# Performance work log

Measured on AMD Instinct MI355X. Metric: run time of the kernel, lower is better.

The kernel has to match this reference:

```python
import jax, jax.numpy as jnp
import numpy as np

DIM = 192
TDIM = 192
HEADS = 6
WS = (2, 7, 7)
SS = (1, 3, 3)
MLP_HID = 4 * DIM
RANK = DIM // 8
EPS = 1e-6


def _rel_pos_index(ws):
    wd, wh, ww = ws
    coords = np.stack(np.meshgrid(np.arange(wd), np.arange(wh), np.arange(ww), indexing='ij'))
    cf = coords.reshape(3, -1)
    rel = (cf[:, :, None] - cf[:, None, :]).transpose(1, 2, 0).astype(np.int64)
    rel[..., 0] += wd - 1
    rel[..., 1] += wh - 1
    rel[..., 2] += ww - 1
    rel[..., 0] *= (2 * wh - 1) * (2 * ww - 1)
    rel[..., 1] *= (2 * ww - 1)
    return rel.sum(-1)  # (N, N)


def _window_partition(x, ws):
    B, D, H, W, C = x.shape
    x = x.reshape(B, D // ws[0], ws[0], H // ws[1], ws[1], W // ws[2], ws[2], C)
    return x.transpose(0, 1, 3, 5, 2, 4, 6, 7).reshape(-1, ws[0] * ws[1] * ws[2], C)


def _window_reverse(w, ws, B, D, H, W):
    x = w.reshape(B, D // ws[0], H // ws[1], W // ws[2], ws[0], ws[1], ws[2], -1)
    return x.transpose(0, 1, 4, 2, 5, 3, 6, 7).reshape(B, D, H, W, -1)


def _ln(x):
    m = x.mean(-1, keepdims=True)
    v = ((x - m) ** 2).mean(-1, keepdims=True)
    return (x - m) * jax.lax.rsqrt(v + EPS)


def _compute_mask_np(Dp, Hp, Wp, ws, ss):
    img = np.zeros((1, Dp, Hp, Wp, 1), dtype=np.float32)
    cnt = 0
    for d in (slice(0, -ws[0]), slice(-ws[0], -ss[0]), slice(-ss[0], None)):
        for h in (slice(0, -ws[1]), slice(-ws[1], -ss[1]), slice(-ss[1], None)):
            for w in (slice(0, -ws[2]), slice(-ws[2], -ss[2]), slice(-ss[2], None)):
                img[:, d, h, w, :] = cnt
                cnt += 1
    x = img.reshape(1, Dp // ws[0], ws[0], Hp // ws[1], ws[1], Wp // ws[2], ws[2], 1)
    mw = x.transpose(0, 1, 3, 5, 2, 4, 6, 7).reshape(-1, ws[0] * ws[1] * ws[2])
    am = mw[:, None, :] - mw[:, :, None]
    return np.where(am != 0, np.float32(-100.0), np.float32(0.0))


def setup_inputs() -> dict:
    key = jax.random.key(0)
    ks = jax.random.split(key, 16)
    B, D, H, W, C = 1, 16, 64, 128, DIM
    Dp = D + (-D) % WS[0]
    Hp = H + (-H) % WS[1]
    Wp = W + (-W) % WS[2]
    s = 0.02
    bias_tab = (2 * WS[0] - 1) * (2 * WS[1] - 1) * (2 * WS[2] - 1)
    return {
        'x': jax.random.normal(ks[0], (B, D, H, W, C), jnp.float32),
        'mask_matrix': jnp.asarray(_compute_mask_np(Dp, Hp, Wp, WS, SS)),
        't': jax.random.normal(ks[1], (B, TDIM), jnp.float32),
        'w_qkv': jax.random.normal(ks[2], (C, 3 * C), jnp.float32) * s,
        'b_qkv': jnp.zeros((3 * C,), jnp.float32),
        'rel_bias': jax.random.normal(ks[3], (bias_tab, HEADS), jnp.float32) * s,
        'w_proj': jax.random.normal(ks[4], (C, C), jnp.float32) * s,
        'b_proj': jnp.zeros((C,), jnp.float32),
        'w1': jax.random.normal(ks[5], (C, MLP_HID), jnp.float32) * s,
        'b1': jnp.zeros((MLP_HID,), jnp.float32),
        'w2': jax.random.normal(ks[6], (MLP_HID, C), jnp.float32) * s,
        'b2': jnp.zeros((C,), jnp.float32),
        'wa1': jax.random.normal(ks[7], (TDIM, RANK), jnp.float32) * s,
        'wa2': jax.random.normal(ks[8], (RANK, 6 * C), jnp.float32) * s,
        'ba2': jax.random.normal(ks[9], (6 * C,), jnp.float32) * s,
    }


def reference(x, mask_matrix, t, w_qkv, b_qkv, rel_bias, w_proj, b_proj, w1, b1, w2, b2, wa1, wa2, ba2):
    B, D, H, W, C = x.shape
    hd = C // HEADS
    # AdaLN modulation params
    mod = (jax.nn.silu(t) @ wa1) @ wa2 + ba2  # (B, 6C)
    sh_msa, sc_msa, g_msa, sh_mlp, sc_mlp, g_mlp = jnp.split(mod, 6, axis=1)

    def modulate(y, sh, sc):
        return y * (1 + sc[:, None, None, None, :]) + sh[:, None, None, None, :]

    shortcut = x
    y = modulate(_ln(x), sh_msa, sc_msa)
    # pad to window multiples
    pad_d, pad_h, pad_w = (-D) % WS[0], (-H) % WS[1], (-W) % WS[2]
    y = jnp.pad(y, ((0, 0), (0, pad_d), (0, pad_h), (0, pad_w), (0, 0)))
    Dp, Hp, Wp = D + pad_d, H + pad_h, W + pad_w
    # cyclic shift
    y = jnp.roll(y, (-SS[0], -SS[1], -SS[2]), axis=(1, 2, 3))
    xw = _window_partition(y, WS)  # (B*nW, N, C)
    N = xw.shape[1]
    qkv = (xw @ w_qkv + b_qkv).reshape(-1, N, 3, HEADS, hd)
    q, k, v = qkv[:, :, 0], qkv[:, :, 1], qkv[:, :, 2]
    scale = hd ** -0.5
    attn = jnp.einsum('bnhd,bmhd->bhnm', q * scale, k)  # (B*nW, H, N, N)
    rpi = _rel_pos_index(WS)
    bias = rel_bias[rpi.reshape(-1)].reshape(N, N, HEADS).transpose(2, 0, 1)
    attn = attn + bias[None]
    nW = mask_matrix.shape[0]
    attn = attn.reshape(B, nW, HEADS, N, N) + mask_matrix[None, :, None]
    attn = jax.nn.softmax(attn, axis=-1).reshape(-1, HEADS, N, N)
    out = jnp.einsum('bhnm,bmhd->bnhd', attn, v).reshape(-1, N, C)
    out = out @ w_proj + b_proj
    y = _window_reverse(out, WS, B, Dp, Hp, Wp)
    y = jnp.roll(y, (SS[0], SS[1], SS[2]), axis=(1, 2, 3))
    y = y[:, :D, :H, :W, :]
    x1 = shortcut + g_msa[:, None, None, None, :] * y
    y2 = modulate(_ln(x1), sh_mlp, sc_mlp)
    h = jax.nn.gelu(y2 @ w1 + b1, approximate=False) @ w2 + b2
    return x1 + g_mlp[:, None, None, None, :] * h
```

## Files before the change

### kernel.cpp

```cpp
#include <hip/hip_runtime.h>
#include <hip/hip_bf16.h>

typedef __bf16 bf16x8 __attribute__((ext_vector_type(8)));
typedef float  f32x4  __attribute__((ext_vector_type(4)));
typedef unsigned int u32x4 __attribute__((ext_vector_type(4)));
typedef __attribute__((address_space(3))) unsigned int lds_u32;
typedef const __attribute__((address_space(1))) unsigned int glb_u32;

__device__ inline unsigned short f2bf(float f) {
    union { __hip_bfloat16 h; unsigned short u; } cv;
    cv.h = __float2bfloat16(f);
    return cv.u;
}
__device__ inline float bf2f(unsigned short u) {
    union { unsigned int i; float f; } c; c.i = ((unsigned int)u) << 16; return c.f;
}

__device__ inline bf16x8 load8(const unsigned short* p) {
    uint2 lo = *(const uint2*)(p);
    uint2 hi = *(const uint2*)(p + 16);
    u32x4 v; v[0] = lo.x; v[1] = lo.y; v[2] = hi.x; v[3] = hi.y;
    return __builtin_bit_cast(bf16x8, v);
}

__device__ inline bf16x8 load8s(const unsigned short* rowbase, int lg, int r3) {
    int b0 = ((((lg >> 1)    ) ^ r3) << 4) + ((lg & 1) << 3);
    int b1 = ((((lg >> 1) + 2) ^ r3) << 4) + ((lg & 1) << 3);
    uint2 lo = *(const uint2*)((const char*)rowbase + b0);
    uint2 hi = *(const uint2*)((const char*)rowbase + b1);
    u32x4 v; v[0] = lo.x; v[1] = lo.y; v[2] = hi.x; v[3] = hi.y;
    return __builtin_bit_cast(bf16x8, v);
}

__device__ inline f32x4 mfma16(bf16x8 a, bf16x8 b, f32x4 c) {
    return __builtin_amdgcn_mfma_f32_16x16x32_bf16(a, b, c, 0, 0, 0);
}

__device__ inline bool winmapT(int gg, int& T) {
    int win = gg / 98, n = gg % 98;
    int wdi = win / 190, rem = win % 190, whi = rem / 19, wwi = rem % 19;
    int td = n / 49, th = (n / 7) % 7, tw = n % 7;
    int sd = (wdi * 2 + td + 1) & 15;
    int sh = whi * 7 + th + 3; if (sh >= 70) sh -= 70;
    int sw = wwi * 7 + tw + 3; if (sw >= 133) sw -= 133;
    if (sh < 64 && sw < 128) { T = (sd * 64 + sh) * 128 + sw; return true; }
    return false;
}

__device__ inline int xcd_swz(int orig, int nwg) {
    int q = nwg >> 3, r = nwg & 7;
    int xcd = orig & 7, idx = orig >> 3;
    return (xcd < r ? xcd * (q + 1) : r * (q + 1) + (xcd - r) * q) + idx;
}

__global__ __launch_bounds__(256) void mod_k(const float* __restrict__ t,
    const float* __restrict__ wa1, const float* __restrict__ wa2,
    const float* __restrict__ ba2, float* __restrict__ mod)
{
    __shared__ float st[192];
    __shared__ float a[24];
    int tid = threadIdx.x;
    if (tid < 192) { float x = t[tid]; st[tid] = x / (1.f + __expf(-x)); }
    __syncthreads();
    if (tid < 24) {
        float s = 0.f;
        for (int c = 0; c < 192; ++c) s += st[c] * wa1[c * 24 + tid];
        a[tid] = s;
    }
    __syncthreads();
    for (int j = tid; j < 1152; j += 256) {
        float s = ba2[j];
        for (int r = 0; r < 24; ++r) s += a[r] * wa2[r * 1152 + j];
        mod[j] = s;
    }
}

__global__ __launch_bounds__(256) void prep_k(
    const float* __restrict__ wqkv, const float* __restrict__ wproj,
    const float* __restrict__ w1, const float* __restrict__ w2,
    const float* __restrict__ relb,
    unsigned short* __restrict__ wqkvT, unsigned short* __restrict__ wprojT,
    unsigned short* __restrict__ w1T, unsigned short* __restrict__ w2T,
    unsigned short* __restrict__ btabF)
{
    int i = blockIdx.x * 256 + threadIdx.x;
    if (i < 110592) { int n = i / 192, k = i % 192; wqkvT[i] = f2bf(wqkv[k * 576 + n]); return; }
    i -= 110592;
    if (i < 36864)  { int n = i / 192, k = i % 192; wprojT[i] = f2bf(wproj[k * 192 + n]); return; }
    i -= 36864;
    if (i < 147456) { int n = i / 192, k = i % 192; w1T[i] = f2bf(w1[k * 768 + n]); return; }
    i -= 147456;
    if (i < 147456) { int n = i / 768, k = i % 768; w2T[i] = f2bf(w2[k * 192 + n]); return; }
    i -= 147456;
    if (i < 688128) {
        int mt = i / 86016, r1 = i % 86016;
        int h  = r1 / 14336, r2 = r1 % 14336;
        int fq = r2 / 2048,  r3 = r2 % 2048;
        int l16 = r3 / 128,  r4 = r3 % 128;
        int lg  = r4 / 32,   r5 = r4 % 32;
        int fkey = r5 / 4,   e  = r5 % 4;
        int q = fq * 16 + l16, key = fkey * 16 + lg * 4 + e;
        float val;
        if (fkey == 7 || q >= 98 || key >= 98) {
            val = -1e30f;
        } else {
            int tdn = q / 49, thn = (q / 7) % 7, twn = q % 7;
            int tdm = key / 49, thm = (key / 7) % 7, twm = key % 7;
            int idx = (tdn - tdm + 1) * 169 + (thn - thm + 6) * 13 + (twn - twm + 6);
            float b = relb[idx * 6 + h];
            int bd = mt & 1, bh = (mt >> 1) & 1, bw = (mt >> 2) & 1;
            int idn = (bd ? (tdn == 0 ? 1 : 2) : 0) * 9 + (bh ? (thn < 4 ? 1 : 2) : 0) * 3 + (bw ? (twn < 4 ? 1 : 2) : 0);
            int idm = (bd ? (tdm == 0 ? 1 : 2) : 0) * 9 + (bh ? (thm < 4 ? 1 : 2) : 0) * 3 + (bw ? (twm < 4 ? 1 : 2) : 0);
            val = b + ((idn != idm) ? -100.f : 0.f);
        }
        btabF[i] = f2bf(val);
    }
}

__global__ __launch_bounds__(256) void lnwin_k(const float* __restrict__ x,
    const float* __restrict__ mod, unsigned short* __restrict__ ywin)
{
    int tok = blockIdx.x * 4 + (threadIdx.x >> 6);
    int lane = threadIdx.x & 63;
    int T;
    size_t ob = (size_t)tok * 192;
    if (winmapT(tok, T)) {
        const float* p = x + (size_t)T * 192;
        float x0 = p[lane], xa = p[64 + lane], xb = p[128 + lane];
        float s = x0 + xa + xb, q = x0 * x0 + xa * xa + xb * xb;
        for (int m = 32; m; m >>= 1) { s += __shfl_xor(s, m); q += __shfl_xor(q, m); }
        float mean = s * (1.f / 192.f);
        float var  = q * (1.f / 192.f) - mean * mean;
        float rstd = rsqrtf(var + 1e-6f);
        ywin[ob + lane]       = f2bf((x0 - mean) * rstd * (1.f + mod[192 + lane])       + mod[lane]);
        ywin[ob + 64 + lane]  = f2bf((xa - mean) * rstd * (1.f + mod[192 + 64 + lane])  + mod[64 + lane]);
        ywin[ob + 128 + lane] = f2bf((xb - mean) * rstd * (1.f + mod[192 + 128 + lane]) + mod[128 + lane]);
    } else {
        ywin[ob + lane] = 0; ywin[ob + 64 + lane] = 0; ywin[ob + 128 + lane] = 0;
    }
}

__global__ __launch_bounds__(256) void ln2_k(const float* __restrict__ x1,
    const float* __restrict__ mod, unsigned short* __restrict__ y2)
{
    int tok = blockIdx.x * 4 + (threadIdx.x >> 6);
    int lane = threadIdx.x & 63;
    const float* p = x1 + (size_t)tok * 192;
    float x0 = p[lane], xa = p[64 + lane], xb = p[128 + lane];
    float s = x0 + xa + xb, q = x0 * x0 + xa * xa + xb * xb;
    for (int m = 32; m; m >>= 1) { s += __shfl_xor(s, m); q += __shfl_xor(q, m); }
    float mean = s * (1.f / 192.f);
    float var  = q * (1.f / 192.f) - mean * mean;
    float rstd = rsqrtf(var + 1e-6f);
    size_t ob = (size_t)tok * 192;
    y2[ob + lane]       = f2bf((x0 - mean) * rstd * (1.f + mod[768 + lane])       + mod[576 + lane]);
    y2[ob + 64 + lane]  = f2bf((xa - mean) * rstd * (1.f + mod[768 + 64 + lane])  + mod[576 + 64 + lane]);
    y2[ob + 128 + lane] = f2bf((xb - mean) * rstd * (1.f + mod[768 + 128 + lane]) + mod[576 + 128 + lane]);
}

template<int FN, int EPI>
__global__ __launch_bounds__(256) void gemm_k(
    const unsigned short* __restrict__ A, const unsigned short* __restrict__ BT,
    const float* __restrict__ bias, unsigned short* __restrict__ outB, float* outF,
    const float* __restrict__ auxF, const float* __restrict__ mod,
    int M, int N, int K, int nx)
{
    constexpr int BN = FN * 32;
    __shared__ unsigned short As[2][128 * 32];
    __shared__ unsigned short Bs[2][BN * 32];
    const int t = threadIdx.x;
    const int wg = xcd_swz(blockIdx.x, gridDim.x);
    const int n0 = (wg % nx) * BN, m0 = (wg / nx) * 128;
    const int wid = t >> 6, lane = t & 63;
    const int lg = lane >> 4, l16 = lane & 15;
    const int wm = (wid >> 1) * 64, wn = (wid & 1) * (FN * 16);
    f32x4 acc[4][FN] = {};

    int arow[2], acs[2];
    #pragma unroll
    for (int j = 0; j < 2; ++j) {
        int p = t + j * 256;
        arow[j] = p >> 2;
        acs[j] = (p & 3) ^ (arow[j] & 3);
    }
    const unsigned short* asrc[2];
    const unsigned short* bsrc[BN / 64];
    #pragma unroll
    for (int j = 0; j < 2; ++j) {
        int gr = m0 + arow[j];
        asrc[j] = A + (size_t)(gr < M ? gr : 0) * K + acs[j] * 8;
    }
    #pragma unroll
    for (int j = 0; j < BN / 64; ++j) {
        int gn = n0 + arow[j];
        bsrc[j] = BT + (size_t)(gn < N ? gn : 0) * K + acs[j] * 8;
    }

    const int NS = K >> 5;

    #pragma unroll
    for (int j = 0; j < 2; ++j)
        __builtin_amdgcn_global_load_lds((glb_u32*)(asrc[j]),
            (lds_u32*)((char*)&As[0][0] + wid * 1024 + j * 4096), 16, 0, 0);
    #pragma unroll
    for (int j = 0; j < BN / 64; ++j)
        __builtin_amdgcn_global_load_lds((glb_u32*)(bsrc[j]),
            (lds_u32*)((char*)&Bs[0][0] + wid * 1024 + j * 4096), 16, 0, 0);
    __syncthreads();

    for (int s = 0; s < NS; ++s) {
        const int cur = s & 1;
        if (s + 1 < NS) {
            const int kk = (s + 1) << 5;
            #pragma unroll
            for (int j = 0; j < 2; ++j)
                __builtin_amdgcn_global_load_lds((glb_u32*)(asrc[j] + kk),
                    (lds_u32*)((char*)&As[cur ^ 1][0] + wid * 1024 + j * 4096), 16, 0, 0);
            #pragma unroll
            for (int j = 0; j < BN / 64; ++j)
                __builtin_amdgcn_global_load_lds((glb_u32*)(bsrc[j] + kk),
                    (lds_u32*)((char*)&Bs[cur ^ 1][0] + wid * 1024 + j * 4096), 16, 0, 0);
        }
        bf16x8 af[4], bv[FN];
        #pragma unroll
        for (int i = 0; i < 4; ++i) {
            int r = wm + i * 16 + l16;
            af[i] = load8s(&As[cur][r * 32], lg, r & 3);
        }
        #pragma unroll
        for (int j = 0; j < FN; ++j) {
            int r = wn + j * 16 + l16;
            bv[j] = load8s(&Bs[cur][r * 32], lg, r & 3);
        }
        #pragma unroll
        for (int i = 0; i < 4; ++i)
        #pragma unroll
        for (int j = 0; j < FN; ++j)
            acc[i][j] = mfma16(af[i], bv[j], acc[i][j]);
        __syncthreads();
    }

    #pragma unroll
    for (int i = 0; i < 4; ++i)
    #pragma unroll
    for (int j = 0; j < FN; ++j) {
        int gcol = n0 + wn + j * 16 + l16;
        if (gcol >= N) continue;
        float b = bias[gcol];
        #pragma unroll
        for (int e = 0; e < 4; ++e) {
            int grow = m0 + wm + i * 16 + lg * 4 + e;
            if (grow >= M) continue;
            float v = acc[i][j][e] + b;
            if (EPI == 0) {
                int which = gcol / 192, hh = (gcol / 32) % 6, c = gcol & 31;
                outB[((size_t)(hh * 3 + which) * 148960 + grow) * 32 + c] = f2bf(v);
            } else if (EPI == 1) {
                float gl = 0.5f * v * (1.f + erff(v * 0.70710678118654752f));
                outB[(size_t)grow * N + gcol] = f2bf(gl);
            } else if (EPI == 2) {
                int T;
                if (winmapT(grow, T)) {
                    size_t idx = (size_t)T * 192 + gcol;
                    outF[idx] = auxF[idx] + mod[384 + gcol] * v;
                }
            } else {
                size_t idx = (size_t)grow * 192 + gcol;
                outF[idx] = outF[idx] + mod[960 + gcol] * v;
            }
        }
    }
}

__global__ __launch_bounds__(256) void attn_k(
    const unsigned short* __restrict__ qkv, const unsigned short* __restrict__ btabF,
    unsigned short* __restrict__ out)
{
    __shared__ __align__(16) unsigned short Ks[2][112 * 46];
    __shared__ __align__(16) unsigned short VT[2][32 * 142];

    const int wg = xcd_swz(blockIdx.x, 4560);
    const int h = wg / 760, wp = wg % 760;
    const int win0 = wp * 2;
    const int t = threadIdx.x;
    const int wid = t >> 6, lg = (t >> 4) & 3, l16 = t & 15;

    const unsigned short* Qg = qkv + (size_t)(h * 3 + 0) * 148960 * 32;
    const unsigned short* Kg = qkv + (size_t)(h * 3 + 1) * 148960 * 32;
    const unsigned short* Vg = qkv + (size_t)(h * 3 + 2) * 148960 * 32;

    const int w2 = wid & 1, fq0 = wid >> 1;
    const int win = win0 + w2;
    const size_t rb = (size_t)win * 98;
    const int wdi = win / 190, remw = win % 190, whi = remw / 19, wwi = remw % 19;
    const int mt = (wdi == 7 ? 1 : 0) | (whi == 9 ? 2 : 0) | (wwi == 18 ? 4 : 0);
    const unsigned short* btW = btabF + (size_t)(mt * 6 + h) * 14336;

    bf16x8 qa[4];
    #pragma unroll
    for (int i = 0; i < 4; ++i) {
        int fq = fq0 + 2 * i;
        int fqc = (fq < 7) ? fq : 0;
        qa[i] = load8(Qg + (rb + fqc * 16 + l16) * 32 + 4 * lg);
    }

    #pragma unroll
    for (int v2 = 0; v2 < 2; ++v2) {
        const size_t rbs = (size_t)(win0 + v2) * 98;
        for (int i = t; i < 392; i += 256) {
            int r = i >> 2, cg = (i & 3) * 8;
            uint4 k = *(const uint4*)(Kg + (rbs + r) * 32 + cg);
            *(uint2*)(&Ks[v2][r * 46 + cg])     = make_uint2(k.x, k.y);
            *(uint2*)(&Ks[v2][r * 46 + cg + 4]) = make_uint2(k.z, k.w);
        }
        for (int i = t; i < 14 * 32; i += 256) {
            int r = 98 + (i >> 5), c = i & 31;
            Ks[v2][r * 46 + c] = 0;
        }
        for (int i = t; i < 512; i += 256) {
            if (i < 392) {
                uint4 v = *(const uint4*)(Vg + (rbs + (i >> 2)) * 32 + (i & 3) * 8);
                const unsigned short* vp = (const unsigned short*)&v;
                int m = i >> 2, c0 = (i & 3) * 8;
                #pragma unroll
                for (int j = 0; j < 8; ++j) VT[v2][(c0 + j) * 142 + m] = vp[j];
            }
        }
        for (int i = t; i < 32 * 30; i += 256) {
            int c = i / 30, m = 98 + i % 30;
            VT[v2][c * 142 + m] = 0;
        }
    }
    __syncthreads();

    __builtin_amdgcn_s_setprio(1);
    const float SCALE = 0.17677669529663687f;
    const unsigned short* KsW = &Ks[w2][0];
    const unsigned short* VTW = &VT[w2][0];

    #pragma unroll
    for (int i = 0; i < 4; ++i) {
        const int fq = fq0 + 2 * i;
        if (fq >= 7) break;

        const uint4* bp = (const uint4*)(btW + fq * 2048 + l16 * 128 + lg * 32);
        uint4 b0 = bp[0], b1 = bp[1], b2 = bp[2], b3 = bp[3];
        const unsigned bt32[16] = {b0.x, b0.y, b0.z, b0.w, b1.x, b1.y, b1.z, b1.w,
                                   b2.x, b2.y, b2.z, b2.w, b3.x, b3.y, b3.z, b3.w};

        f32x4 acc[7];
        #pragma unroll
        for (int fk = 0; fk < 7; ++fk) {
            bf16x8 kb = load8(KsW + (fk * 16 + l16) * 46 + 4 * lg);
            f32x4 z = {};
            acc[fk] = mfma16(kb, qa[i], z);
        }

        float mx = -1e30f;
        #pragma unroll
        for (int fk = 0; fk < 7; ++fk)
        #pragma unroll
        for (int e = 0; e < 4; ++e) {
            unsigned short bu = (unsigned short)(bt32[fk * 2 + (e >> 1)] >> ((e & 1) * 16));
            float s = fmaf(acc[fk][e], SCALE, bf2f(bu));
            acc[fk][e] = s;
            mx = fmaxf(mx, s);
        }
        mx = fmaxf(mx, __shfl_xor(mx, 16));
        mx = fmaxf(mx, __shfl_xor(mx, 32));
        float sum = 0.f;
        #pragma unroll
        for (int fk = 0; fk < 7; ++fk)
        #pragma unroll
        for (int e = 0; e < 4; ++e) {
            float p = __expf(acc[fk][e] - mx);
            acc[fk][e] = p;
            sum += p;
        }
        sum += __shfl_xor(sum, 16);
        sum += __shfl_xor(sum, 32);
        float rinv = 1.f / sum;

        bf16x8 sa[4];
        #pragma unroll
        for (int ks = 0; ks < 4; ++ks) {
            u32x4 w;
            w[0] = (unsigned)f2bf(acc[2 * ks][0]) | ((unsigned)f2bf(acc[2 * ks][1]) << 16);
            w[1] = (unsigned)f2bf(acc[2 * ks][2]) | ((unsigned)f2bf(acc[2 * ks][3]) << 16);
            if (ks < 3) {
                w[2] = (unsigned)f2bf(acc[2 * ks + 1][0]) | ((unsigned)f2bf(acc[2 * ks + 1][1]) << 16);
                w[3] = (unsigned)f2bf(acc[2 * ks + 1][2]) | ((unsigned)f2bf(acc[2 * ks + 1][3]) << 16);
            } else {
                w[2] = 0u; w[3] = 0u;
            }
            sa[ks] = __builtin_bit_cast(bf16x8, w);
        }
        float rv[4];
        #pragma unroll
        for (int e = 0; e < 4; ++e) rv[e] = __shfl(rinv, lg * 4 + e);

        #pragma unroll
        for (int fn = 0; fn < 2; ++fn) {
            f32x4 o = {};
            #pragma unroll
            for (int ks = 0; ks < 4; ++ks) {
                bf16x8 vb = load8(VTW + (fn * 16 + l16) * 142 + ks * 32 + 4 * lg);
                o = mfma16(sa[ks], vb, o);
            }
            #pragma unroll
            for (int e = 0; e < 4; ++e) {
                int r = fq * 16 + lg * 4 + e;
                if (r < 98) {
                    out[(rb + r) * 192 + h * 32 + fn * 16 + l16] = f2bf(o[e] * rv[e]);
                }
            }
        }
    }
    __builtin_amdgcn_s_setprio(0);
}

extern "C" void kernel_launch(void* const* d_in, const int* in_sizes, int n_in,
                              void* d_out, int out_size, void* d_ws, size_t ws_size,
                              hipStream_t stream)
{
    const float* x      = (const float*)d_in[0];
    const float* tvec   = (const float*)d_in[2];
    const float* w_qkv  = (const float*)d_in[3];
    const float* b_qkv  = (const float*)d_in[4];
    const float* relb   = (const float*)d_in[5];
    const float* w_proj = (const float*)d_in[6];
    const float* b_proj = (const float*)d_in[7];
    const float* w1     = (const float*)d_in[8];
    const float* b1     = (const float*)d_in[9];
    const float* w2     = (const float*)d_in[10];
    const float* b2     = (const float*)d_in[11];
    const float* wa1    = (const float*)d_in[12];
    const float* wa2    = (const float*)d_in[13];
    const float* ba2    = (const float*)d_in[14];

    char* ws = (char*)d_ws;
    float*          mod    = (float*)ws;
    unsigned short* wqkvT  = (unsigned short*)(ws + 2101760);
    unsigned short* wprojT = (unsigned short*)(ws + 2322944);
    unsigned short* w1T    = (unsigned short*)(ws + 2396672);
    unsigned short* w2T    = (unsigned short*)(ws + 2691584);
    unsigned short* btabF  = (unsigned short*)(ws + 2986496);
    unsigned short* qkvb   = (unsigned short*)(ws + 4834304);
    unsigned short* h      = (unsigned short*)(ws + 4834304);
    unsigned short* attn_c = (unsigned short*)(ws + 176436224);
    unsigned short* ywin   = (unsigned short*)(ws + 233636864);
    unsigned short* y2b    = (unsigned short*)(ws + 290837504);
    float*          dout   = (float*)d_out;

    mod_k<<<1, 256, 0, stream>>>(tvec, wa1, wa2, ba2, mod);
    prep_k<<<4416, 256, 0, stream>>>(w_qkv, w_proj, w1, w2, relb, wqkvT, wprojT, w1T, w2T, btabF);
    lnwin_k<<<37240, 256, 0, stream>>>(x, mod, ywin);

    gemm_k<4, 0><<<5 * 1164, 256, 0, stream>>>(
        ywin, wqkvT, b_qkv, qkvb, nullptr, nullptr, mod, 148960, 576, 192, 5);
    attn_k<<<4560, 256, 0, stream>>>(qkvb, btabF, attn_c);
    gemm_k<2, 2><<<3 * 1164, 256, 0, stream>>>(
        attn_c, wprojT, b_proj, nullptr, dout, x, mod, 148960, 192, 192, 3);

    ln2_k<<<32768, 256, 0, stream>>>(dout, mod, y2b);

    gemm_k<4, 1><<<6 * 1024, 256, 0, stream>>>(
        y2b, w1T, b1, h, nullptr, nullptr, mod, 131072, 768, 192, 6);
    gemm_k<2, 3><<<3 * 1024, 256, 0, stream>>>(
        h, w2T, b2, nullptr, dout, nullptr, mod, 131072, 192, 768, 3);
}
```

Measured before the change: 928.8 us.

## Fuse QKV projection into window attention kernel, one block per window

Replaces the separate QKV GEMM and attention kernels with one kernel per window. It loads the window's 98 tokens into LDS, computes Q/K/V per head with MFMA against head-reordered weights, and runs attention directly from LDS. This removes the global round trip of the large QKV intermediate. The trade-offs are heavy LDS use, which lowers occupancy, only 1520 blocks, serialized per-head work inside each block, and weights reloaded from global memory for every window.

```diff
diff --git a/kernel.cpp b/kernel.cpp
--- a/kernel.cpp
+++ b/kernel.cpp
@@ -76,15 +76,22 @@
 }
 
 __global__ __launch_bounds__(256) void prep_k(
-    const float* __restrict__ wqkv, const float* __restrict__ wproj,
+    const float* __restrict__ wqkv, const float* __restrict__ bqkv,
+    const float* __restrict__ wproj,
     const float* __restrict__ w1, const float* __restrict__ w2,
     const float* __restrict__ relb,
-    unsigned short* __restrict__ wqkvT, unsigned short* __restrict__ wprojT,
+    unsigned short* __restrict__ wqkvH, float* __restrict__ bqkvH,
+    unsigned short* __restrict__ wprojT,
     unsigned short* __restrict__ w1T, unsigned short* __restrict__ w2T,
     unsigned short* __restrict__ btabF)
 {
     int i = blockIdx.x * 256 + threadIdx.x;
-    if (i < 110592) { int n = i / 192, k = i % 192; wqkvT[i] = f2bf(wqkv[k * 576 + n]); return; }
+    if (i < 110592) {
+        int h = i / 18432, r = i % 18432, c96 = r / 192, k = r % 192;
+        int which = c96 >> 5, c = c96 & 31;
+        wqkvH[i] = f2bf(wqkv[k * 576 + which * 192 + h * 32 + c]);
+        return;
+    }
     i -= 110592;
     if (i < 36864)  { int n = i / 192, k = i % 192; wprojT[i] = f2bf(wproj[k * 192 + n]); return; }
     i -= 36864;
@@ -114,6 +121,13 @@
             val = b + ((idn != idm) ? -100.f : 0.f);
         }
         btabF[i] = f2bf(val);
+        return;
+    }
+    i -= 688128;
+    if (i < 576) {
+        int h = i / 96, c96 = i % 96;
+        int which = c96 >> 5, c = c96 & 31;
+        bqkvH[i] = bqkv[which * 192 + h * 32 + c];
     }
 }
 
@@ -252,10 +266,7 @@
             int grow = m0 + wm + i * 16 + lg * 4 + e;
             if (grow >= M) continue;
             float v = acc[i][j][e] + b;
-            if (EPI == 0) {
-                int which = gcol / 192, hh = (gcol / 32) % 6, c = gcol & 31;
-                outB[((size_t)(hh * 3 + which) * 148960 + grow) * 32 + c] = f2bf(v);
-            } else if (EPI == 1) {
+            if (EPI == 1) {
                 float gl = 0.5f * v * (1.f + erff(v * 0.70710678118654752f));
                 outB[(size_t)grow * N + gcol] = f2bf(gl);
             } else if (EPI == 2) {
@@ -272,151 +283,164 @@
     }
 }
 
-__global__ __launch_bounds__(256) void attn_k(
-    const unsigned short* __restrict__ qkv, const unsigned short* __restrict__ btabF,
+__global__ __launch_bounds__(256) void qkvattn_k(
+    const unsigned short* __restrict__ ywin, const unsigned short* __restrict__ wqkvH,
+    const float* __restrict__ bqkvH, const unsigned short* __restrict__ btabF,
     unsigned short* __restrict__ out)
 {
-    __shared__ __align__(16) unsigned short Ks[2][112 * 46];
-    __shared__ __align__(16) unsigned short VT[2][32 * 142];
-
-    const int wg = xcd_swz(blockIdx.x, 4560);
-    const int h = wg / 760, wp = wg % 760;
-    const int win0 = wp * 2;
+    __shared__ unsigned short As[128 * 196];
+    __shared__ unsigned short Bs[96 * 196];
+    __shared__ unsigned short Qs[112 * 46];
+    __shared__ unsigned short Ks[112 * 46];
+    __shared__ unsigned short VT[32 * 142];
+
+    const int win = xcd_swz(blockIdx.x, 1520);
     const int t = threadIdx.x;
-    const int wid = t >> 6, lg = (t >> 4) & 3, l16 = t & 15;
-
-    const unsigned short* Qg = qkv + (size_t)(h * 3 + 0) * 148960 * 32;
-    const unsigned short* Kg = qkv + (size_t)(h * 3 + 1) * 148960 * 32;
-    const unsigned short* Vg = qkv + (size_t)(h * 3 + 2) * 148960 * 32;
-
-    const int w2 = wid & 1, fq0 = wid >> 1;
-    const int win = win0 + w2;
+    const int wid = t >> 6, lane = t & 63;
+    const int lg = lane >> 4, l16 = lane & 15;
+    const int wr = wid >> 1, wc = wid & 1;
     const size_t rb = (size_t)win * 98;
+
     const int wdi = win / 190, remw = win % 190, whi = remw / 19, wwi = remw % 19;
     const int mt = (wdi == 7 ? 1 : 0) | (whi == 9 ? 2 : 0) | (wwi == 18 ? 4 : 0);
-    const unsigned short* btW = btabF + (size_t)(mt * 6 + h) * 14336;
-
-    bf16x8 qa[4];
-    #pragma unroll
-    for (int i = 0; i < 4; ++i) {
-        int fq = fq0 + 2 * i;
-        int fqc = (fq < 7) ? fq : 0;
-        qa[i] = load8(Qg + (rb + fqc * 16 + l16) * 32 + 4 * lg);
-    }
-
-    #pragma unroll
-    for (int v2 = 0; v2 < 2; ++v2) {
-        const size_t rbs = (size_t)(win0 + v2) * 98;
-        for (int i = t; i < 392; i += 256) {
-            int r = i >> 2, cg = (i & 3) * 8;
-            uint4 k = *(const uint4*)(Kg + (rbs + r) * 32 + cg);
-            *(uint2*)(&Ks[v2][r * 46 + cg])     = make_uint2(k.x, k.y);
-            *(uint2*)(&Ks[v2][r * 46 + cg + 4]) = make_uint2(k.z, k.w);
-        }
-        for (int i = t; i < 14 * 32; i += 256) {
-            int r = 98 + (i >> 5), c = i & 31;
-            Ks[v2][r * 46 + c] = 0;
-        }
-        for (int i = t; i < 512; i += 256) {
-            if (i < 392) {
-                uint4 v = *(const uint4*)(Vg + (rbs + (i >> 2)) * 32 + (i & 3) * 8);
-                const unsigned short* vp = (const unsigned short*)&v;
-                int m = i >> 2, c0 = (i & 3) * 8;
+    const float SCALE = 0.17677669529663687f;
+
+    for (int p = t; p < 128 * 24; p += 256) {
+        int row = p / 24, ch = p % 24;
+        uint4 w = make_uint4(0u, 0u, 0u, 0u);
+        if (row < 98) w = *(const uint4*)(ywin + (rb + row) * 192 + ch * 8);
+        *(uint2*)(&As[row * 196 + ch * 8])     = make_uint2(w.x, w.y);
+        *(uint2*)(&As[row * 196 + ch * 8 + 4]) = make_uint2(w.z, w.w);
+    }
+
+    for (int h = 0; h < 6; ++h) {
+        const unsigned short* Wh = wqkvH + (size_t)h * 96 * 192;
+        for (int p = t; p < 96 * 24; p += 256) {
+            int row = p / 24, ch = p % 24;
+            uint4 w = *(const uint4*)(Wh + row * 192 + ch * 8);
+            *(uint2*)(&Bs[row * 196 + ch * 8])     = make_uint2(w.x, w.y);
+            *(uint2*)(&Bs[row * 196 + ch * 8 + 4]) = make_uint2(w.z, w.w);
+        }
+        __syncthreads();
+
+        __builtin_amdgcn_s_setprio(1);
+        f32x4 acc[4][3] = {};
+        #pragma unroll
+        for (int kb = 0; kb < 6; ++kb) {
+            bf16x8 af[4], bv[3];
+            #pragma unroll
+            for (int i2 = 0; i2 < 4; ++i2)
+                af[i2] = load8(&As[(wr * 64 + i2 * 16 + l16) * 196 + kb * 32 + 4 * lg]);
+            #pragma unroll
+            for (int j = 0; j < 3; ++j)
+                bv[j] = load8(&Bs[(wc * 48 + j * 16 + l16) * 196 + kb * 32 + 4 * lg]);
+            #pragma unroll
+            for (int i2 = 0; i2 < 4; ++i2)
+            #pragma unroll
+            for (int j = 0; j < 3; ++j)
+                acc[i2][j] = mfma16(af[i2], bv[j], acc[i2][j]);
+        }
+        __builtin_amdgcn_s_setprio(0);
+
+        #pragma unroll
+        for (int j = 0; j < 3; ++j) {
+            int c96 = wc * 48 + j * 16 + l16;
+            float bb = bqkvH[h * 96 + c96];
+            int which = c96 >> 5, c = c96 & 31;
+            #pragma unroll
+            for (int i2 = 0; i2 < 4; ++i2)
+            #pragma unroll
+            for (int e = 0; e < 4; ++e) {
+                int row = wr * 64 + i2 * 16 + lg * 4 + e;
+                unsigned short val = f2bf(acc[i2][j][e] + bb);
+                if (which == 0)      { if (row < 112) Qs[row * 46 + c] = val; }
+                else if (which == 1) { if (row < 112) Ks[row * 46 + c] = val; }
+                else                 { VT[c * 142 + row] = val; }
+            }
+        }
+        __syncthreads();
+
+        const unsigned short* btW = btabF + (size_t)(mt * 6 + h) * 14336;
+        #pragma unroll
+        for (int fi = 0; fi < 2; ++fi) {
+            const int fq = wid + fi * 4;
+            if (fq >= 7) break;
+
+            const uint4* bp = (const uint4*)(btW + fq * 2048 + l16 * 128 + lg * 32);
+            uint4 b0 = bp[0], b1 = bp[1], b2 = bp[2], b3 = bp[3];
+            const unsigned bt32[16] = {b0.x, b0.y, b0.z, b0.w, b1.x, b1.y, b1.z, b1.w,
+                                       b2.x, b2.y, b2.z, b2.w, b3.x, b3.y, b3.z, b3.w};
+
+            bf16x8 qa = load8(Qs + (fq * 16 + l16) * 46 + 4 * lg);
+            f32x4 sc[7];
+            #pragma unroll
+            for (int fk = 0; fk < 7; ++fk) {
+                bf16x8 kb = load8(Ks + (fk * 16 + l16) * 46 + 4 * lg);
+                f32x4 z = {};
+                sc[fk] = mfma16(kb, qa, z);
+            }
+
+            float mx = -1e30f;
+            #pragma unroll
+            for (int fk = 0; fk < 7; ++fk)
+            #pragma unroll
+            for (int e = 0; e < 4; ++e) {
+                unsigned short bu = (unsigned short)(bt32[fk * 2 + (e >> 1)] >> ((e & 1) * 16));
+                float s = fmaf(sc[fk][e], SCALE, bf2f(bu));
+                sc[fk][e] = s;
+                mx = fmaxf(mx, s);
+            }
+            mx = fmaxf(mx, __shfl_xor(mx, 16));
+            mx = fmaxf(mx, __shfl_xor(mx, 32));
+            float sum = 0.f;
+            #pragma unroll
+            for (int fk = 0; fk < 7; ++fk)
+            #pragma unroll
+            for (int e = 0; e < 4; ++e) {
+                float p = __expf(sc[fk][e] - mx);
+                sc[fk][e] = p;
+                sum += p;
+            }
+            sum += __shfl_xor(sum, 16);
+            sum += __shfl_xor(sum, 32);
+            float rinv = 1.f / sum;
+
+            bf16x8 sa[4];
+            #pragma unroll
+            for (int ks = 0; ks < 4; ++ks) {
+                u32x4 w;
+                w[0] = (unsigned)f2bf(sc[2 * ks][0]) | ((unsigned)f2bf(sc[2 * ks][1]) << 16);
+                w[1] = (unsigned)f2bf(sc[2 * ks][2]) | ((unsigned)f2bf(sc[2 * ks][3]) << 16);
+                if (ks < 3) {
+                    w[2] = (unsigned)f2bf(sc[2 * ks + 1][0]) | ((unsigned)f2bf(sc[2 * ks + 1][1]) << 16);
+                    w[3] = (unsigned)f2bf(sc[2 * ks + 1][2]) | ((unsigned)f2bf(sc[2 * ks + 1][3]) << 16);
+                } else {
+                    w[2] = 0u; w[3] = 0u;
+                }
+                sa[ks] = __builtin_bit_cast(bf16x8, w);
+            }
+            float rv[4];
+            #pragma unroll
+            for (int e = 0; e < 4; ++e) rv[e] = __shfl(rinv, lg * 4 + e);
+
+            #pragma unroll
+            for (int fn = 0; fn < 2; ++fn) {
+                f32x4 o = {};
                 #pragma unroll
-                for (int j = 0; j < 8; ++j) VT[v2][(c0 + j) * 142 + m] = vp[j];
-            }
-        }
-        for (int i = t; i < 32 * 30; i += 256) {
-            int c = i / 30, m = 98 + i % 30;
-            VT[v2][c * 142 + m] = 0;
-        }
-    }
-    __syncthreads();
-
-    __builtin_amdgcn_s_setprio(1);
-    const float SCALE = 0.17677669529663687f;
-    const unsigned short* KsW = &Ks[w2][0];
-    const unsigned short* VTW = &VT[w2][0];
-
-    #pragma unroll
-    for (int i = 0; i < 4; ++i) {
-        const int fq = fq0 + 2 * i;
-        if (fq >= 7) break;
-
-        const uint4* bp = (const uint4*)(btW + fq * 2048 + l16 * 128 + lg * 32);
-        uint4 b0 = bp[0], b1 = bp[1], b2 = bp[2], b3 = bp[3];
-        const unsigned bt32[16] = {b0.x, b0.y, b0.z, b0.w, b1.x, b1.y, b1.z, b1.w,
-                                   b2.x, b2.y, b2.z, b2.w, b3.x, b3.y, b3.z, b3.w};
-
-        f32x4 acc[7];
-        #pragma unroll
-        for (int fk = 0; fk < 7; ++fk) {
-            bf16x8 kb = load8(KsW + (fk * 16 + l16) * 46 + 4 * lg);
-            f32x4 z = {};
-            acc[fk] = mfma16(kb, qa[i], z);
-        }
-
-        float mx = -1e30f;
-        #pragma unroll
-        for (int fk = 0; fk < 7; ++fk)
-        #pragma unroll
-        for (int e = 0; e < 4; ++e) {
-            unsigned short bu = (unsigned short)(bt32[fk * 2 + (e >> 1)] >> ((e & 1) * 16));
-            float s = fmaf(acc[fk][e], SCALE, bf2f(bu));
-            acc[fk][e] = s;
-            mx = fmaxf(mx, s);
-        }
-        mx = fmaxf(mx, __shfl_xor(mx, 16));
-        mx = fmaxf(mx, __shfl_xor(mx, 32));
-        float sum = 0.f;
-        #pragma unroll
-        for (int fk = 0; fk < 7; ++fk)
-        #pragma unroll
-        for (int e = 0; e < 4; ++e) {
-            float p = __expf(acc[fk][e] - mx);
-            acc[fk][e] = p;
-            sum += p;
-        }
-        sum += __shfl_xor(sum, 16);
-        sum += __shfl_xor(sum, 32);
-        float rinv = 1.f / sum;
-
-        bf16x8 sa[4];
-        #pragma unroll
-        for (int ks = 0; ks < 4; ++ks) {
-            u32x4 w;
-            w[0] = (unsigned)f2bf(acc[2 * ks][0]) | ((unsigned)f2bf(acc[2 * ks][1]) << 16);
-            w[1] = (unsigned)f2bf(acc[2 * ks][2]) | ((unsigned)f2bf(acc[2 * ks][3]) << 16);
-            if (ks < 3) {
-                w[2] = (unsigned)f2bf(acc[2 * ks + 1][0]) | ((unsigned)f2bf(acc[2 * ks + 1][1]) << 16);
-                w[3] = (unsigned)f2bf(acc[2 * ks + 1][2]) | ((unsigned)f2bf(acc[2 * ks + 1][3]) << 16);
-            } else {
-                w[2] = 0u; w[3] = 0u;
-            }
-            sa[ks] = __builtin_bit_cast(bf16x8, w);
-        }
-        float rv[4];
-        #pragma unroll
-        for (int e = 0; e < 4; ++e) rv[e] = __shfl(rinv, lg * 4 + e);
-
-        #pragma unroll
-        for (int fn = 0; fn < 2; ++fn) {
-            f32x4 o = {};
-            #pragma unroll
-            for (int ks = 0; ks < 4; ++ks) {
-                bf16x8 vb = load8(VTW + (fn * 16 + l16) * 142 + ks * 32 + 4 * lg);
-                o = mfma16(sa[ks], vb, o);
-            }
-            #pragma unroll
-            for (int e = 0; e < 4; ++e) {
-                int r = fq * 16 + lg * 4 + e;
-                if (r < 98) {
-                    out[(rb + r) * 192 + h * 32 + fn * 16 + l16] = f2bf(o[e] * rv[e]);
+                for (int ks = 0; ks < 4; ++ks) {
+                    bf16x8 vb = load8(VT + (fn * 16 + l16) * 142 + ks * 32 + 4 * lg);
+                    o = mfma16(sa[ks], vb, o);
                 }
-            }
-        }
-    }
-    __builtin_amdgcn_s_setprio(0);
+                #pragma unroll
+                for (int e = 0; e < 4; ++e) {
+                    int r = fq * 16 + lg * 4 + e;
+                    if (r < 98) {
+                        out[(rb + r) * 192 + h * 32 + fn * 16 + l16] = f2bf(o[e] * rv[e]);
+                    }
+                }
+            }
+        }
+    }
 }
 
 extern "C" void kernel_launch(void* const* d_in, const int* in_sizes, int n_in,
@@ -440,12 +464,12 @@
 
     char* ws = (char*)d_ws;
     float*          mod    = (float*)ws;
-    unsigned short* wqkvT  = (unsigned short*)(ws + 2101760);
+    float*          bqkvH  = (float*)(ws + 4608);
+    unsigned short* wqkvH  = (unsigned short*)(ws + 2101760);
     unsigned short* wprojT = (unsigned short*)(ws + 2322944);
     unsigned short* w1T    = (unsigned short*)(ws + 2396672);
     unsigned short* w2T    = (unsigned short*)(ws + 2691584);
     unsigned short* btabF  = (unsigned short*)(ws + 2986496);
-    unsigned short* qkvb   = (unsigned short*)(ws + 4834304);
     unsigned short* h      = (unsigned short*)(ws + 4834304);
     unsigned short* attn_c = (unsigned short*)(ws + 176436224);
     unsigned short* ywin   = (unsigned short*)(ws + 233636864);
@@ -453,12 +477,11 @@
     float*          dout   = (float*)d_out;
 
     mod_k<<<1, 256, 0, stream>>>(tvec, wa1, wa2, ba2, mod);
-    prep_k<<<4416, 256, 0, stream>>>(w_qkv, w_proj, w1, w2, relb, wqkvT, wprojT, w1T, w2T, btabF);
+    prep_k<<<4418, 256, 0, stream>>>(w_qkv, b_qkv, w_proj, w1, w2, relb,
+                                     wqkvH, bqkvH, wprojT, w1T, w2T, btabF);
     lnwin_k<<<37240, 256, 0, stream>>>(x, mod, ywin);
 
-    gemm_k<4, 0><<<5 * 1164, 256, 0, stream>>>(
-        ywin, wqkvT, b_qkv, qkvb, nullptr, nullptr, mod, 148960, 576, 192, 5);
-    attn_k<<<4560, 256, 0, stream>>>(qkvb, btabF, attn_c);
+    qkvattn_k<<<1520, 256, 0, stream>>>(ywin, wqkvH, bqkvH, btabF, attn_c);
     gemm_k<2, 2><<<3 * 1164, 256, 0, stream>>>(
         attn_c, wprojT, b_proj, nullptr, dout, x, mod, 148960, 192, 192, 3);
 
```

Result: slower. 1.005 ms (+8.2%).
